# Kernel optimization log

Hardware: AMD Instinct MI355X
Metric: run time of the kernel (lower is better)

The kernel has to match this reference:

```python
import jax, jax.numpy as jnp
import numpy as np

BS = 4
EMBED = 256
HEADS = 8
LEVELS = 4
POINTS = 4
HD = EMBED // HEADS  # 32
SHAPES = np.array([[96, 96], [48, 48], [24, 24], [12, 12]], dtype=np.int64)
LQ = int((SHAPES[:, 0] * SHAPES[:, 1]).sum())  # 12240


def _offset_bias():
    # faithful to MSDeformableAttention._reset_parameters grid init
    thetas = np.arange(HEADS, dtype=np.float32) * (2.0 * np.pi / HEADS)
    g = np.stack([np.cos(thetas), np.sin(thetas)], -1)
    g = g / np.abs(g).max(-1, keepdims=True)
    g = np.tile(g.reshape(HEADS, 1, 1, 2), (1, LEVELS, POINTS, 1))
    g = g * np.arange(1, POINTS + 1, dtype=np.float32).reshape(1, 1, -1, 1)
    return jnp.asarray(g.reshape(-1), dtype=jnp.float32)


def setup_inputs() -> dict:
    key = jax.random.key(0)
    ks = jax.random.split(key, 8)
    tp = HEADS * LEVELS * POINTS
    d = {}
    d["query"] = jax.random.normal(ks[0], (BS, LQ, EMBED), jnp.float32)
    d["reference_points"] = jax.random.uniform(ks[1], (BS, LQ, LEVELS, 2), jnp.float32)
    d["value"] = jax.random.normal(ks[2], (BS, LQ, EMBED), jnp.float32)
    d["value_spatial_shapes"] = SHAPES  # static numpy, int
    d["W_off"] = jax.random.normal(ks[3], (EMBED, tp * 2), jnp.float32) * 0.01
    d["b_off"] = _offset_bias()
    d["W_attn"] = jax.random.normal(ks[4], (EMBED, tp), jnp.float32) * 0.02
    d["b_attn"] = jnp.zeros((tp,), jnp.float32)
    d["W_val"] = jax.random.normal(ks[5], (EMBED, EMBED), jnp.float32) * (1.0 / np.sqrt(EMBED).astype(np.float32))
    d["b_val"] = jnp.zeros((EMBED,), jnp.float32)
    d["W_out"] = jax.random.normal(ks[6], (EMBED, EMBED), jnp.float32) * (1.0 / np.sqrt(EMBED).astype(np.float32))
    d["b_out"] = jnp.zeros((EMBED,), jnp.float32)
    return d


def _bilinear_sample(img, grid):
    # img: [B,H,W,C]; grid: [B,Q,P,2] in [-1,1] (x,y)
    # matches F.grid_sample(mode='bilinear', padding_mode='zeros', align_corners=False)
    B, H, W, C = img.shape
    gx = (grid[..., 0] + 1.0) * (W * 0.5) - 0.5
    gy = (grid[..., 1] + 1.0) * (H * 0.5) - 0.5
    x0 = jnp.floor(gx)
    y0 = jnp.floor(gy)
    wx = gx - x0
    wy = gy - y0
    x0i = x0.astype(jnp.int32)
    y0i = y0.astype(jnp.int32)
    x1i = x0i + 1
    y1i = y0i + 1
    flat = img.reshape(B, H * W, C)

    def corner(xi, yi, w):
        valid = (xi >= 0) & (xi < W) & (yi >= 0) & (yi < H)
        idx = jnp.clip(yi, 0, H - 1) * W + jnp.clip(xi, 0, W - 1)
        v = jnp.take_along_axis(flat, idx.reshape(B, -1, 1), axis=1)
        v = v.reshape(idx.shape + (C,))
        return v * (w * valid)[..., None]

    return (corner(x0i, y0i, (1.0 - wx) * (1.0 - wy))
            + corner(x1i, y0i, wx * (1.0 - wy))
            + corner(x0i, y1i, (1.0 - wx) * wy)
            + corner(x1i, y1i, wx * wy))


def reference(query, reference_points, value, value_spatial_shapes,
              W_off, b_off, W_attn, b_attn, W_val, b_val, W_out, b_out):
    shapes = np.asarray(value_spatial_shapes)  # static [L,2] (H,W)
    bs, Lq, _ = query.shape
    v = (value @ W_val + b_val).reshape(bs, -1, HEADS, HD)  # [bs,Lv,H,hd]
    off = (query @ W_off + b_off).reshape(bs, Lq, HEADS, LEVELS, POINTS, 2)
    aw = jax.nn.softmax((query @ W_attn + b_attn).reshape(bs, Lq, HEADS, LEVELS * POINTS), axis=-1)
    aw = aw.reshape(bs, Lq, HEADS, LEVELS, POINTS)
    # normalizer is (W,H) per level
    norm = jnp.asarray(shapes[:, ::-1].copy(), jnp.float32).reshape(1, 1, 1, LEVELS, 1, 2)
    loc = reference_points[:, :, None, :, None, :] + off / norm
    grids = 2.0 * loc - 1.0  # [bs,Lq,H,L,P,2]

    acc = jnp.zeros((bs * HEADS, Lq, HD), query.dtype)
    start = 0
    for lvl in range(LEVELS):
        h, w = int(shapes[lvl, 0]), int(shapes[lvl, 1])
        v_l = v[:, start:start + h * w].reshape(bs, h, w, HEADS, HD)
        v_l = v_l.transpose(0, 3, 1, 2, 4).reshape(bs * HEADS, h, w, HD)
        g_l = grids[:, :, :, lvl].transpose(0, 2, 1, 3, 4).reshape(bs * HEADS, Lq, POINTS, 2)
        s_l = _bilinear_sample(v_l, g_l)  # [bs*H, Lq, P, hd]
        w_l = aw[:, :, :, lvl].transpose(0, 2, 1, 3).reshape(bs * HEADS, Lq, POINTS)
        acc = acc + jnp.einsum('bqpc,bqp->bqc', s_l, w_l)
        start += h * w

    out = acc.reshape(bs, HEADS, Lq, HD).transpose(0, 2, 1, 3).reshape(bs, Lq, EMBED)
    return out @ W_out + b_out
```

## Files before the change

kernel.cpp:

```cpp
#include <hip/hip_runtime.h>
#include <hip/hip_bf16.h>

static constexpr int BS     = 4;
static constexpr int EMBED  = 256;
static constexpr int HEADS  = 8;
static constexpr int LEVELS = 4;
static constexpr int POINTS = 4;
static constexpr int HD     = 32;
static constexpr int LQ     = 12240;
static constexpr int NROW   = BS * LQ;
static constexpr int LVL_W[4]  = {96, 48, 24, 12};
static constexpr int LVL_H[4]  = {96, 48, 24, 12};
static constexpr int LVL_ST[4] = {0, 9216, 11520, 12096};

typedef __attribute__((ext_vector_type(8))) short short8;
typedef __attribute__((ext_vector_type(4))) float f32x4;
typedef __attribute__((ext_vector_type(2))) float f32x2;

__device__ __forceinline__ unsigned short f2bf(float f) {
    unsigned int u = __float_as_uint(f);
    unsigned int r = (u + 0x7FFFu + ((u >> 16) & 1u)) >> 16;
    return (unsigned short)r;
}

__device__ __forceinline__ void pkfma(f32x2& a, f32x2 v, f32x2 w) {
    asm("v_pk_fma_f32 %0, %1, %2, %0" : "+v"(a) : "v"(v), "v"(w));
}

__global__ __launch_bounds__(256) void prep_weights(
    const float* __restrict__ W_off, const float* __restrict__ W_attn,
    const float* __restrict__ W_val, const float* __restrict__ W_out,
    unsigned short* __restrict__ WT_oa, unsigned short* __restrict__ WT_val,
    unsigned short* __restrict__ WT_out)
{
    const int gid = blockIdx.x * 256 + threadIdx.x;
    const int k = gid & 255;
    const int n = gid >> 8;
    if (n < 384) {
        const float v = (n < 256) ? W_off[k * 256 + n] : W_attn[k * 128 + (n - 256)];
        WT_oa[n * 256 + k] = f2bf(v);
    } else if (n < 640) {
        const int nn = n - 384;
        WT_val[nn * 256 + k] = f2bf(W_val[k * 256 + nn]);
    } else {
        const int nn = n - 640;
        WT_out[nn * 256 + k] = f2bf(W_out[k * 256 + nn]);
    }
}

template <int NTW, bool A_BF16, bool OUT_BF16>
__global__ __launch_bounds__(256) void gemm_mfma(
    const void* __restrict__ Av, const unsigned short* __restrict__ Wt,
    const float* __restrict__ bias0, const float* __restrict__ bias1, int nsplit,
    void* __restrict__ Cv, int N)
{
    constexpr int NB = NTW * 64;
    constexpr int K  = 256;
    __shared__ __align__(16) unsigned short As[64][40];
    __shared__ __align__(16) unsigned short Bs[NB][40];

    const int tid = threadIdx.x;
    const int m0 = blockIdx.y * 64;
    const int n0 = blockIdx.x * NB;
    const int w  = tid >> 6;
    const int l  = tid & 63;
    const int lm = l & 15;
    const int lq = l >> 4;

    const int sr = tid >> 2;
    const int kg = (tid & 3) * 8;

    float4 pa0, pa1; short8 pa_bf;
    short8 pb[NTW];

    auto gload = [&](int k0) {
        if (A_BF16) {
            const unsigned short* A = (const unsigned short*)Av;
            pa_bf = *(const short8*)&A[(size_t)(m0 + sr) * K + k0 + kg];
        } else {
            const float* A = (const float*)Av;
            const float* ap = &A[(size_t)(m0 + sr) * K + k0 + kg];
            pa0 = *(const float4*)ap;
            pa1 = *(const float4*)(ap + 4);
        }
        #pragma unroll
        for (int i = 0; i < NTW; ++i) {
            const int slot = tid + i * 256;
            const int n  = slot >> 2;
            const int kk = (slot & 3) * 8;
            pb[i] = *(const short8*)&Wt[(size_t)(n0 + n) * K + k0 + kk];
        }
    };

    f32x4 acc[4][NTW];
    #pragma unroll
    for (int rg = 0; rg < 4; ++rg)
        #pragma unroll
        for (int nt = 0; nt < NTW; ++nt)
            acc[rg][nt] = (f32x4){0.f, 0.f, 0.f, 0.f};

    gload(0);
    #pragma unroll 2
    for (int k0 = 0; k0 < K; k0 += 32) {
        if (A_BF16) {
            *(short8*)&As[sr][kg] = pa_bf;
        } else {
            uint4 pk;
            pk.x = (unsigned int)f2bf(pa0.x) | ((unsigned int)f2bf(pa0.y) << 16);
            pk.y = (unsigned int)f2bf(pa0.z) | ((unsigned int)f2bf(pa0.w) << 16);
            pk.z = (unsigned int)f2bf(pa1.x) | ((unsigned int)f2bf(pa1.y) << 16);
            pk.w = (unsigned int)f2bf(pa1.z) | ((unsigned int)f2bf(pa1.w) << 16);
            *(uint4*)&As[sr][kg] = pk;
        }
        #pragma unroll
        for (int i = 0; i < NTW; ++i) {
            const int slot = tid + i * 256;
            const int n  = slot >> 2;
            const int kk = (slot & 3) * 8;
            *(short8*)&Bs[n][kk] = pb[i];
        }
        __syncthreads();

        if (k0 + 32 < K) gload(k0 + 32);

        short8 af[4];
        #pragma unroll
        for (int rg = 0; rg < 4; ++rg)
            af[rg] = *(const short8*)&As[rg * 16 + lm][lq * 8];
        #pragma unroll
        for (int nt = 0; nt < NTW; ++nt) {
            const short8 bf = *(const short8*)&Bs[(w * NTW + nt) * 16 + lm][lq * 8];
            #pragma unroll
            for (int rg = 0; rg < 4; ++rg)
                acc[rg][nt] = __builtin_amdgcn_mfma_f32_16x16x32_bf16(af[rg], bf, acc[rg][nt], 0, 0, 0);
        }
        __syncthreads();
    }

    #pragma unroll
    for (int nt = 0; nt < NTW; ++nt) {
        const int col = n0 + (w * NTW + nt) * 16 + lm;
        const float b = (col < nsplit) ? bias0[col] : bias1[col - nsplit];
        #pragma unroll
        for (int rg = 0; rg < 4; ++rg)
            #pragma unroll
            for (int r = 0; r < 4; ++r) {
                const int row = m0 + rg * 16 + lq * 4 + r;
                const float v = acc[rg][nt][r] + b;
                if (OUT_BF16) ((unsigned short*)Cv)[(size_t)row * N + col] = f2bf(v);
                else          ((float*)Cv)[(size_t)row * N + col] = v;
            }
    }
}

__global__ __launch_bounds__(256, 8) void sample_kernel(
    const unsigned short* __restrict__ V,
    const float* __restrict__ OA,
    const float* __restrict__ refp,
    unsigned short* __restrict__ ACC)
{
    __shared__ __align__(16) unsigned int pr_o[512][4];
    __shared__ __align__(16) unsigned int pr_w[512][4];

    const int tid = threadIdx.x;

    {
        const int g = tid & 31;
        const int r = g >> 3;
        const int h = g & 7;
        const int L = tid >> 5;
        const int prow = blockIdx.x * 4 + r;
        const float* rowp = OA + (size_t)prow * 384;

        const float lg0 = rowp[256 + h * 16 + L];
        const float lg1 = rowp[256 + h * 16 + L + 8];

        float* smax = (float*)pr_w;
        float* ssum = smax + 264;
        smax[L * 33 + g] = fmaxf(lg0, lg1);
        __syncthreads();
        float m = smax[g];
        #pragma unroll
        for (int k = 1; k < 8; ++k) m = fmaxf(m, smax[k * 33 + g]);
        const float e0 = __expf(lg0 - m);
        const float e1 = __expf(lg1 - m);
        ssum[L * 33 + g] = e0 + e1;
        __syncthreads();
        float sden = ssum[g];
        #pragma unroll
        for (int k = 1; k < 8; ++k) sden += ssum[k * 33 + g];
        const float inv = 1.0f / sden;

        uint4 wstash[2];
        int   sidx[2];
        #pragma unroll
        for (int ss = 0; ss < 2; ++ss) {
            const int lp  = L + ss * 8;
            const int s   = lp * 32 + g;
            const int lvl = lp >> 2;
            const int Wl = LVL_W[lvl], Hl = LVL_H[lvl], st = LVL_ST[lvl];

            const float2 oxy = *(const float2*)&rowp[h * 32 + lp * 2];
            const float2 rxy = *(const float2*)&refp[(size_t)prow * 8 + lvl * 2];
            const float wgt = (ss ? e1 : e0) * inv;

            const float gx = (rxy.x + oxy.x / (float)Wl) * (float)Wl - 0.5f;
            const float gy = (rxy.y + oxy.y / (float)Hl) * (float)Hl - 0.5f;

            const float fx = floorf(gx), fy = floorf(gy);
            const float wx = gx - fx,    wy = gy - fy;
            const int x0 = (int)fx, y0 = (int)fy;
            const int x1 = x0 + 1,  y1 = y0 + 1;

            const bool bx0 = ((unsigned)x0 < (unsigned)Wl);
            const bool bx1 = ((unsigned)x1 < (unsigned)Wl);
            const bool by0 = ((unsigned)y0 < (unsigned)Hl);
            const bool by1 = ((unsigned)y1 < (unsigned)Hl);
            const float w00 = (bx0 && by0) ? (1.f - wx) * (1.f - wy) * wgt : 0.f;
            const float w10 = (bx1 && by0) ? wx * (1.f - wy) * wgt : 0.f;
            const float w01 = (bx0 && by1) ? (1.f - wx) * wy * wgt : 0.f;
            const float w11 = (bx1 && by1) ? wx * wy * wgt : 0.f;

            const int cx0 = min(max(x0, 0), Wl - 1);
            const int cx1 = min(max(x1, 0), Wl - 1);
            const int cy0 = min(max(y0, 0), Hl - 1);
            const int cy1 = min(max(y1, 0), Hl - 1);

            uint4 o;
            o.x = (unsigned int)(st + cy0 * Wl + cx0) * 512u;
            o.y = (unsigned int)(st + cy0 * Wl + cx1) * 512u;
            o.z = (unsigned int)(st + cy1 * Wl + cx0) * 512u;
            o.w = (unsigned int)(st + cy1 * Wl + cx1) * 512u;
            *(uint4*)&pr_o[s][0] = o;

            uint4 wv;
            wv.x = __float_as_uint(w00); wv.y = __float_as_uint(w10);
            wv.z = __float_as_uint(w01); wv.w = __float_as_uint(w11);
            wstash[ss] = wv;
            sidx[ss] = s;
        }
        __syncthreads();
        *(uint4*)&pr_w[sidx[0]][0] = wstash[0];
        *(uint4*)&pr_w[sidx[1]][0] = wstash[1];
    }
    __syncthreads();

    const int w    = tid >> 6;
    const int l    = tid & 63;
    const int half = l >> 5;
    const int head = (l >> 2) & 7;
    const int c16  = (l & 3) * 16;

    const int row  = __builtin_amdgcn_readfirstlane(blockIdx.x * 4 + w);
    const int b    = row / LQ;
    const char* vrow = (const char*)V + (size_t)b * ((size_t)LQ * 512);
    const unsigned int lane_byte = (unsigned int)(head * 64 + c16);
    const int sid0 = half * 256 + w * 8 + head;

    uint4 dat[2][4];
    f32x2 accA[4], accB[4];
    #pragma unroll
    for (int i = 0; i < 4; ++i) { accA[i] = (f32x2){0.f,0.f}; accB[i] = (f32x2){0.f,0.f}; }

    auto ldissue = [&](int j, int buf) {
        const uint4 o = *(const uint4*)&pr_o[sid0 + j * 32][0];
        dat[buf][0] = *(const uint4*)(vrow + (lane_byte + o.x));
        dat[buf][1] = *(const uint4*)(vrow + (lane_byte + o.y));
        dat[buf][2] = *(const uint4*)(vrow + (lane_byte + o.z));
        dat[buf][3] = *(const uint4*)(vrow + (lane_byte + o.w));
    };
    auto pkstep = [&](f32x2& A, f32x2& B, unsigned u0, unsigned u1, f32x2 w2) {
        f32x2 pa, pb;
        pa.x = __uint_as_float(u0 << 16);
        pa.y = __uint_as_float(u1 << 16);
        pb.x = __uint_as_float(u0 & 0xffff0000u);
        pb.y = __uint_as_float(u1 & 0xffff0000u);
        pkfma(A, pa, w2);
        pkfma(B, pb, w2);
    };
    auto consume = [&](int j, int buf) {
        const f32x4 wv = *(const f32x4*)&pr_w[sid0 + j * 32][0];
        f32x2 w01; w01.x = wv.x; w01.y = wv.y;
        f32x2 w23; w23.x = wv.z; w23.y = wv.w;
        const uint4 d0 = dat[buf][0], d1 = dat[buf][1];
        pkstep(accA[0], accB[0], d0.x, d1.x, w01);
        pkstep(accA[1], accB[1], d0.y, d1.y, w01);
        pkstep(accA[2], accB[2], d0.z, d1.z, w01);
        pkstep(accA[3], accB[3], d0.w, d1.w, w01);
        const uint4 d2 = dat[buf][2], d3 = dat[buf][3];
        pkstep(accA[0], accB[0], d2.x, d3.x, w23);
        pkstep(accA[1], accB[1], d2.y, d3.y, w23);
        pkstep(accA[2], accB[2], d2.z, d3.z, w23);
        pkstep(accA[3], accB[3], d2.w, d3.w, w23);
    };

    ldissue(0, 0);
    #pragma unroll
    for (int j = 0; j < 8; ++j) {
        if (j < 7) ldissue(j + 1, (j + 1) & 1);
        consume(j, j & 1);
    }

    float c[8];
    #pragma unroll
    for (int i = 0; i < 4; ++i) {
        c[2 * i]     = accA[i].x + accA[i].y;
        c[2 * i + 1] = accB[i].x + accB[i].y;
    }
    #pragma unroll
    for (int i = 0; i < 8; ++i) c[i] += __shfl_xor(c[i], 32);

    if (half == 0) {
        uint4 o;
        o.x = (unsigned int)f2bf(c[0]) | ((unsigned int)f2bf(c[1]) << 16);
        o.y = (unsigned int)f2bf(c[2]) | ((unsigned int)f2bf(c[3]) << 16);
        o.z = (unsigned int)f2bf(c[4]) | ((unsigned int)f2bf(c[5]) << 16);
        o.w = (unsigned int)f2bf(c[6]) | ((unsigned int)f2bf(c[7]) << 16);
        *(uint4*)((char*)(ACC + (size_t)row * EMBED) + head * 64 + c16) = o;
    }
}

extern "C" void kernel_launch(void* const* d_in, const int* in_sizes, int n_in,
                              void* d_out, int out_size, void* d_ws, size_t ws_size,
                              hipStream_t stream) {
    const float* query  = (const float*)d_in[0];
    const float* refp   = (const float*)d_in[1];
    const float* value  = (const float*)d_in[2];
    const float* W_off  = (const float*)d_in[4];
    const float* b_off  = (const float*)d_in[5];
    const float* W_attn = (const float*)d_in[6];
    const float* b_attn = (const float*)d_in[7];
    const float* W_val  = (const float*)d_in[8];
    const float* b_val  = (const float*)d_in[9];
    const float* W_out  = (const float*)d_in[10];
    const float* b_out  = (const float*)d_in[11];
    float* out = (float*)d_out;

    unsigned short* WT_oa  = (unsigned short*)d_ws;
    unsigned short* WT_val = WT_oa  + 384 * 256;
    unsigned short* WT_out = WT_val + 256 * 256;
    unsigned short* V      = WT_out + 256 * 256;
    float*          OA     = (float*)(V + (size_t)NROW * EMBED);
    unsigned short* ACCb   = (unsigned short*)(OA + (size_t)NROW * 384);

    dim3 blk(256);

    prep_weights<<<896, blk, 0, stream>>>(W_off, W_attn, W_val, W_out,
                                          WT_oa, WT_val, WT_out);
    gemm_mfma<4, false, true><<<dim3(1, NROW / 64), blk, 0, stream>>>(
        value, WT_val, b_val, b_val, 256, V, 256);
    gemm_mfma<3, false, false><<<dim3(2, NROW / 64), blk, 0, stream>>>(
        query, WT_oa, b_off, b_attn, 256, OA, 384);
    sample_kernel<<<NROW / 4, blk, 0, stream>>>(V, OA, refp, ACCb);
    gemm_mfma<4, true, false><<<dim3(1, NROW / 64), blk, 0, stream>>>(
        ACCb, WT_out, b_out, b_out, 256, out, 256);
}
```

Before: 368.3 us.

## Merge value and offset GEMMs, remap sample blocks per XCD, stage OA rows in LDS

```diff
diff --git a/kernel.cpp b/kernel.cpp
--- a/kernel.cpp
+++ b/kernel.cpp
@@ -48,8 +48,112 @@
     }
 }
 
+__global__ __launch_bounds__(256, 5) void gemm_vo(
+    const float* __restrict__ Aval, const float* __restrict__ Aqry,
+    const unsigned short* __restrict__ Wval, const unsigned short* __restrict__ Woa,
+    const float* __restrict__ bval, const float* __restrict__ boff,
+    const float* __restrict__ battn,
+    unsigned short* __restrict__ Vout, float* __restrict__ OAout)
+{
+    constexpr int NTW = 2;
+    constexpr int NB  = 128;
+    constexpr int K   = 256;
+    __shared__ __align__(16) unsigned short As[64][40];
+    __shared__ __align__(16) unsigned short Bs[NB][40];
+
+    const int x    = blockIdx.x;
+    const bool isV = (x < 2);
+    const float* A = isV ? Aval : Aqry;
+    const unsigned short* Wt = isV ? Wval : Woa;
+    const int n0   = isV ? x * 128 : (x - 2) * 128;
+
+    const int tid = threadIdx.x;
+    const int m0 = blockIdx.y * 64;
+    const int w  = tid >> 6;
+    const int l  = tid & 63;
+    const int lm = l & 15;
+    const int lq = l >> 4;
+
+    const int sr = tid >> 2;
+    const int kg = (tid & 3) * 8;
+
+    float4 pa0, pa1;
+    short8 pb[NTW];
+
+    auto gload = [&](int k0) {
+        const float* ap = &A[(size_t)(m0 + sr) * K + k0 + kg];
+        pa0 = *(const float4*)ap;
+        pa1 = *(const float4*)(ap + 4);
+        #pragma unroll
+        for (int i = 0; i < NTW; ++i) {
+            const int slot = tid + i * 256;
+            const int n  = slot >> 2;
+            const int kk = (slot & 3) * 8;
+            pb[i] = *(const short8*)&Wt[(size_t)(n0 + n) * K + k0 + kk];
+        }
+    };
+
+    f32x4 acc[4][NTW];
+    #pragma unroll
+    for (int rg = 0; rg < 4; ++rg)
+        #pragma unroll
+        for (int nt = 0; nt < NTW; ++nt)
+            acc[rg][nt] = (f32x4){0.f, 0.f, 0.f, 0.f};
+
+    gload(0);
+    #pragma unroll 2
+    for (int k0 = 0; k0 < K; k0 += 32) {
+        uint4 pk;
+        pk.x = (unsigned int)f2bf(pa0.x) | ((unsigned int)f2bf(pa0.y) << 16);
+        pk.y = (unsigned int)f2bf(pa0.z) | ((unsigned int)f2bf(pa0.w) << 16);
+        pk.z = (unsigned int)f2bf(pa1.x) | ((unsigned int)f2bf(pa1.y) << 16);
+        pk.w = (unsigned int)f2bf(pa1.z) | ((unsigned int)f2bf(pa1.w) << 16);
+        *(uint4*)&As[sr][kg] = pk;
+        #pragma unroll
+        for (int i = 0; i < NTW; ++i) {
+            const int slot = tid + i * 256;
+            const int n  = slot >> 2;
+            const int kk = (slot & 3) * 8;
+            *(short8*)&Bs[n][kk] = pb[i];
+        }
+        __syncthreads();
+
+        if (k0 + 32 < K) gload(k0 + 32);
+
+        short8 af[4];
+        #pragma unroll
+        for (int rg = 0; rg < 4; ++rg)
+            af[rg] = *(const short8*)&As[rg * 16 + lm][lq * 8];
+        #pragma unroll
+        for (int nt = 0; nt < NTW; ++nt) {
+            const short8 bf = *(const short8*)&Bs[(w * NTW + nt) * 16 + lm][lq * 8];
+            #pragma unroll
+            for (int rg = 0; rg < 4; ++rg)
+                acc[rg][nt] = __builtin_amdgcn_mfma_f32_16x16x32_bf16(af[rg], bf, acc[rg][nt], 0, 0, 0);
+        }
+        __syncthreads();
+    }
+
+    #pragma unroll
+    for (int nt = 0; nt < NTW; ++nt) {
+        const int col = n0 + (w * NTW + nt) * 16 + lm;
+        float b;
+        if (isV) b = bval[col];
+        else     b = (col < 256) ? boff[col] : battn[col - 256];
+        #pragma unroll
+        for (int rg = 0; rg < 4; ++rg)
+            #pragma unroll
+            for (int r = 0; r < 4; ++r) {
+                const int row = m0 + rg * 16 + lq * 4 + r;
+                const float v = acc[rg][nt][r] + b;
+                if (isV) Vout[(size_t)row * 256 + col] = f2bf(v);
+                else     OAout[(size_t)row * 384 + col] = v;
+            }
+    }
+}
+
 template <int NTW, bool A_BF16, bool OUT_BF16>
-__global__ __launch_bounds__(256) void gemm_mfma(
+__global__ __launch_bounds__(256, 5) void gemm_mfma(
     const void* __restrict__ Av, const unsigned short* __restrict__ Wt,
     const float* __restrict__ bias0, const float* __restrict__ bias1, int nsplit,
     void* __restrict__ Cv, int N)
@@ -153,7 +257,7 @@
     }
 }
 
-__global__ __launch_bounds__(256, 8) void sample_kernel(
+__global__ __launch_bounds__(256, 6) void sample_kernel(
     const unsigned short* __restrict__ V,
     const float* __restrict__ OA,
     const float* __restrict__ refp,
@@ -164,13 +268,25 @@
 
     const int tid = threadIdx.x;
 
+    const unsigned bx = blockIdx.x;
+    const int xcd  = bx & 7;
+    const int slot = bx >> 3;
+    const int batch = xcd >> 1;
+    const int wb   = slot * 2 + (xcd & 1);
+    const int row0 = batch * LQ + wb * 4;
+
     {
+        float4* dst = (float4*)pr_o;
+        const float4* src = (const float4*)(OA + (size_t)row0 * 384);
+        dst[tid] = src[tid];
+        if (tid < 128) dst[tid + 256] = src[tid + 256];
+        __syncthreads();
+
         const int g = tid & 31;
         const int r = g >> 3;
         const int h = g & 7;
         const int L = tid >> 5;
-        const int prow = blockIdx.x * 4 + r;
-        const float* rowp = OA + (size_t)prow * 384;
+        const float* rowp = (const float*)pr_o + r * 384;
 
         const float lg0 = rowp[256 + h * 16 + L];
         const float lg1 = rowp[256 + h * 16 + L + 8];
@@ -191,7 +307,7 @@
         for (int k = 1; k < 8; ++k) sden += ssum[k * 33 + g];
         const float inv = 1.0f / sden;
 
-        uint4 wstash[2];
+        uint4 ostash[2], wstash[2];
         int   sidx[2];
         #pragma unroll
         for (int ss = 0; ss < 2; ++ss) {
@@ -201,7 +317,7 @@
             const int Wl = LVL_W[lvl], Hl = LVL_H[lvl], st = LVL_ST[lvl];
 
             const float2 oxy = *(const float2*)&rowp[h * 32 + lp * 2];
-            const float2 rxy = *(const float2*)&refp[(size_t)prow * 8 + lvl * 2];
+            const float2 rxy = *(const float2*)&refp[(size_t)(row0 + r) * 8 + lvl * 2];
             const float wgt = (ss ? e1 : e0) * inv;
 
             const float gx = (rxy.x + oxy.x / (float)Wl) * (float)Wl - 0.5f;
@@ -231,7 +347,7 @@
             o.y = (unsigned int)(st + cy0 * Wl + cx1) * 512u;
             o.z = (unsigned int)(st + cy1 * Wl + cx0) * 512u;
             o.w = (unsigned int)(st + cy1 * Wl + cx1) * 512u;
-            *(uint4*)&pr_o[s][0] = o;
+            ostash[ss] = o;
 
             uint4 wv;
             wv.x = __float_as_uint(w00); wv.y = __float_as_uint(w10);
@@ -240,6 +356,8 @@
             sidx[ss] = s;
         }
         __syncthreads();
+        *(uint4*)&pr_o[sidx[0]][0] = ostash[0];
+        *(uint4*)&pr_o[sidx[1]][0] = ostash[1];
         *(uint4*)&pr_w[sidx[0]][0] = wstash[0];
         *(uint4*)&pr_w[sidx[1]][0] = wstash[1];
     }
@@ -251,23 +369,28 @@
     const int head = (l >> 2) & 7;
     const int c16  = (l & 3) * 16;
 
-    const int row  = __builtin_amdgcn_readfirstlane(blockIdx.x * 4 + w);
-    const int b    = row / LQ;
-    const char* vrow = (const char*)V + (size_t)b * ((size_t)LQ * 512);
+    const int row  = __builtin_amdgcn_readfirstlane(row0 + w);
+    const char* vrow = (const char*)V + (size_t)batch * ((size_t)LQ * 512);
     const unsigned int lane_byte = (unsigned int)(head * 64 + c16);
     const int sid0 = half * 256 + w * 8 + head;
 
+    uint4 ofs[2];
+    f32x4 wv[2];
     uint4 dat[2][4];
     f32x2 accA[4], accB[4];
     #pragma unroll
     for (int i = 0; i < 4; ++i) { accA[i] = (f32x2){0.f,0.f}; accB[i] = (f32x2){0.f,0.f}; }
 
-    auto ldissue = [&](int j, int buf) {
-        const uint4 o = *(const uint4*)&pr_o[sid0 + j * 32][0];
+    auto ldglb = [&](int buf) {
+        const uint4 o = ofs[buf];
         dat[buf][0] = *(const uint4*)(vrow + (lane_byte + o.x));
         dat[buf][1] = *(const uint4*)(vrow + (lane_byte + o.y));
         dat[buf][2] = *(const uint4*)(vrow + (lane_byte + o.z));
         dat[buf][3] = *(const uint4*)(vrow + (lane_byte + o.w));
+    };
+    auto ldpr = [&](int j, int buf) {
+        ofs[buf] = *(const uint4*)&pr_o[sid0 + j * 32][0];
+        wv[buf]  = *(const f32x4*)&pr_w[sid0 + j * 32][0];
     };
     auto pkstep = [&](f32x2& A, f32x2& B, unsigned u0, unsigned u1, f32x2 w2) {
         f32x2 pa, pb;
@@ -278,10 +401,9 @@
         pkfma(A, pa, w2);
         pkfma(B, pb, w2);
     };
-    auto consume = [&](int j, int buf) {
-        const f32x4 wv = *(const f32x4*)&pr_w[sid0 + j * 32][0];
-        f32x2 w01; w01.x = wv.x; w01.y = wv.y;
-        f32x2 w23; w23.x = wv.z; w23.y = wv.w;
+    auto consume = [&](int buf) {
+        f32x2 w01; w01.x = wv[buf].x; w01.y = wv[buf].y;
+        f32x2 w23; w23.x = wv[buf].z; w23.y = wv[buf].w;
         const uint4 d0 = dat[buf][0], d1 = dat[buf][1];
         pkstep(accA[0], accB[0], d0.x, d1.x, w01);
         pkstep(accA[1], accB[1], d0.y, d1.y, w01);
@@ -294,11 +416,14 @@
         pkstep(accA[3], accB[3], d2.w, d3.w, w23);
     };
 
-    ldissue(0, 0);
+    ldpr(0, 0);
+    ldpr(1, 1);
+    ldglb(0);
     #pragma unroll
     for (int j = 0; j < 8; ++j) {
-        if (j < 7) ldissue(j + 1, (j + 1) & 1);
-        consume(j, j & 1);
+        if (j + 1 < 8) ldglb((j + 1) & 1);
+        consume(j & 1);
+        if (j + 2 < 8) ldpr(j + 2, j & 1);
     }
 
     float c[8];
@@ -347,11 +472,9 @@
 
     prep_weights<<<896, blk, 0, stream>>>(W_off, W_attn, W_val, W_out,
                                           WT_oa, WT_val, WT_out);
-    gemm_mfma<4, false, true><<<dim3(1, NROW / 64), blk, 0, stream>>>(
-        value, WT_val, b_val, b_val, 256, V, 256);
-    gemm_mfma<3, false, false><<<dim3(2, NROW / 64), blk, 0, stream>>>(
-        query, WT_oa, b_off, b_attn, 256, OA, 384);
+    gemm_vo<<<dim3(5, NROW / 64), blk, 0, stream>>>(
+        value, query, WT_val, WT_oa, b_val, b_off, b_attn, V, OA);
     sample_kernel<<<NROW / 4, blk, 0, stream>>>(V, OA, refp, ACCb);
-    gemm_mfma<4, true, false><<<dim3(1, NROW / 64), blk, 0, stream>>>(
+    gemm_mfma<2, true, false><<<dim3(2, NROW / 64), blk, 0, stream>>>(
         ACCb, WT_out, b_out, b_out, 256, out, 256);
 }
```

Measured after the change: 332.3 us. 9.8% less time.
